# Performance work log

Measured on AMD Instinct MI355X. Metric: run time of the kernel, lower is better.

The kernel has to match this reference:

```python
import jax, jax.numpy as jnp
import numpy as np

DT = 0.01
NJ = 7
GRAV = 9.81
Q_LOWER = jnp.array([-2.9671, -1.8326, -2.9671, -3.1416, -2.9671, -0.0873, -2.9671], jnp.float32)
Q_UPPER = jnp.array([ 2.9671,  1.8326,  2.9671,  0.0,     2.9671,  3.8223,  2.9671], jnp.float32)


def _skew(v):
    z = jnp.zeros((), v.dtype)
    return jnp.stack([jnp.stack([z, -v[2], v[1]]),
                      jnp.stack([v[2], z, -v[0]]),
                      jnp.stack([-v[1], v[0], z])])


def _mot_X(E, r):
    # 6x6 spatial motion transform [[E,0],[-E*skew(r),E]]
    zero = jnp.zeros_like(E)
    top = jnp.concatenate([E, zero], axis=1)
    bot = jnp.concatenate([-E @ _skew(r), E], axis=1)
    return jnp.concatenate([top, bot], axis=0)


def _crm(v):
    # spatial motion cross-product matrix for v=[w;v0]
    Sw, Sv = _skew(v[:3]), _skew(v[3:])
    zero = jnp.zeros_like(Sw)
    top = jnp.concatenate([Sw, zero], axis=1)
    bot = jnp.concatenate([Sv, Sw], axis=1)
    return jnp.concatenate([top, bot], axis=0)


def _step_single(x, u, axes, R_tree, p_tree, I_sp):
    dt_ = x.dtype
    q = jnp.clip(x[:NJ], Q_LOWER.astype(dt_), Q_UPPER.astype(dt_))
    qd = x[NJ:]
    # forward kinematics: per-joint 6x6 child<-parent transforms and motion subspaces
    Xups, Ss = [], []
    eye3 = jnp.eye(3, dtype=dt_)
    for i in range(NJ):
        a = axes[i]
        c, s = jnp.cos(q[i]), jnp.sin(q[i])
        R = c * eye3 + s * _skew(a) + (1.0 - c) * jnp.outer(a, a)  # rodrigues
        Xj = _mot_X(R.T, jnp.zeros(3, dt_))
        Xt = _mot_X(R_tree[i], p_tree[i])
        Xups.append(Xj @ Xt)
        Ss.append(jnp.concatenate([a, jnp.zeros(3, dt_)]))
    # RNEA bias force h (qdd=0, gravity, zero base velocity, identity base pose)
    v_prev = jnp.zeros(6, dt_)
    a_prev = jnp.array([0.0, 0.0, 0.0, 0.0, 0.0, GRAV], dt_)  # a_base = -g trick
    fs = []
    for i in range(NJ):
        vJ = Ss[i] * qd[i]
        v = Xups[i] @ v_prev + vJ
        acc = Xups[i] @ a_prev + _crm(v) @ vJ
        Iv = I_sp[i] @ v
        f = I_sp[i] @ acc - _crm(v).T @ Iv  # crf(v) = -crm(v)^T
        fs.append(f)
        v_prev, a_prev = v, acc
    h = [None] * NJ
    for i in range(NJ - 1, -1, -1):
        h[i] = Ss[i] @ fs[i]
        if i > 0:
            fs[i - 1] = fs[i - 1] + Xups[i].T @ fs[i]
    h = jnp.stack(h)
    # CRBA mass matrix (serial chain, parent(i)=i-1)
    Ic = [I_sp[i] for i in range(NJ)]
    M = jnp.zeros((NJ, NJ), dt_)
    for i in range(NJ - 1, -1, -1):
        if i > 0:
            Ic[i - 1] = Ic[i - 1] + Xups[i].T @ Ic[i] @ Xups[i]
        F = Ic[i] @ Ss[i]
        M = M.at[i, i].set(Ss[i] @ F)
        for j in range(i - 1, -1, -1):
            F = Xups[j + 1].T @ F
            mij = Ss[j] @ F
            M = M.at[i, j].set(mij).at[j, i].set(mij)
    M = M + 1e-8 * jnp.eye(NJ, dtype=dt_)
    qdd = jnp.linalg.solve(M, (u - h)[:, None])[:, 0]
    qd_new = qd + DT * qdd
    q_new = q + DT * qd_new
    return jnp.concatenate([q_new, qd_new])


def setup_inputs() -> dict:
    B = 65536
    key = jax.random.key(0)
    k1, k2 = jax.random.split(key)
    x = jax.random.normal(k1, (B, 14), jnp.float32)
    u = jax.random.normal(k2, (B, 7), jnp.float32)
    rng = np.random.default_rng(0)
    # unit joint axes
    axes = rng.normal(size=(NJ, 3))
    axes = axes / np.linalg.norm(axes, axis=1, keepdims=True)
    # orthonormal fixed parent->child rotations (det +1)
    R_tree = np.empty((NJ, 3, 3))
    for i in range(NJ):
        Q, _ = np.linalg.qr(rng.normal(size=(3, 3)))
        if np.linalg.det(Q) < 0:
            Q[:, 0] = -Q[:, 0]
        R_tree[i] = Q
    p_tree = 0.2 * rng.normal(size=(NJ, 3))
    # SPD 6x6 spatial inertias: [[Ibar, m*Cx],[m*Cx^T, m*I3]]
    I_sp = np.empty((NJ, 6, 6))
    for i in range(NJ):
        m = float(rng.uniform(1.0, 5.0))
        c = 0.05 * rng.normal(size=3)
        Cx = np.array([[0, -c[2], c[1]], [c[2], 0, -c[0]], [-c[1], c[0], 0]])
        A = 0.1 * rng.normal(size=(3, 3))
        Ic_ = A @ A.T + 0.05 * np.eye(3)
        Ibar = Ic_ + m * Cx @ Cx.T
        I_sp[i] = np.block([[Ibar, m * Cx], [m * Cx.T, m * np.eye(3)]])
    return {
        "x": x, "u": u,
        "axes": jnp.asarray(axes, jnp.float32),
        "R_tree": jnp.asarray(R_tree, jnp.float32),
        "p_tree": jnp.asarray(p_tree, jnp.float32),
        "I_sp": jnp.asarray(I_sp, jnp.float32),
    }


def reference(x, u, axes, R_tree, p_tree, I_sp):
    return jax.vmap(_step_single, in_axes=(0, 0, None, None, None, None))(
        x, u, axes, R_tree, p_tree, I_sp)
```

## Files before the change

kernel.cpp:

```cpp
#include <hip/hip_runtime.h>
#include <math.h>

#define NJ 7
#define DTF 0.01f
#define GRAVF 9.81f
#define MIX(i,j) ((i)*((i)+1)/2 + (j))
#define MPAD 29
#define CW 44


__device__ __forceinline__ void cross3(const float* a, const float* b, float* o){
    o[0] = a[1]*b[2] - a[2]*b[1];
    o[1] = a[2]*b[0] - a[0]*b[2];
    o[2] = a[0]*b[1] - a[1]*b[0];
}
__device__ __forceinline__ void mv3(const float* E, const float* x, float* y){
    y[0] = E[0]*x[0] + E[1]*x[1] + E[2]*x[2];
    y[1] = E[3]*x[0] + E[4]*x[1] + E[5]*x[2];
    y[2] = E[6]*x[0] + E[7]*x[1] + E[8]*x[2];
}
__device__ __forceinline__ void mtv3(const float* E, const float* x, float* y){
    y[0] = E[0]*x[0] + E[3]*x[1] + E[6]*x[2];
    y[1] = E[1]*x[0] + E[4]*x[1] + E[7]*x[2];
    y[2] = E[2]*x[0] + E[5]*x[1] + E[8]*x[2];
}
__device__ __forceinline__ void symv(const float* S, const float* x, float* y){
    y[0] = S[0]*x[0] + S[1]*x[1] + S[2]*x[2];
    y[1] = S[1]*x[0] + S[3]*x[1] + S[4]*x[2];
    y[2] = S[2]*x[0] + S[4]*x[1] + S[5]*x[2];
}
__device__ __forceinline__ void mm3(const float* A, const float* B, float* o){
#pragma unroll
    for (int r = 0; r < 3; r++)
#pragma unroll
        for (int c = 0; c < 3; c++)
            o[r*3+c] = A[r*3]*B[c] + A[r*3+1]*B[3+c] + A[r*3+2]*B[6+c];
}
__device__ __forceinline__ void congr(const float* E, const float* X, float* o){
    float t[9];
#pragma unroll
    for (int r = 0; r < 3; r++)
#pragma unroll
        for (int c = 0; c < 3; c++)
            t[r*3+c] = E[r]*X[c] + E[3+r]*X[3+c] + E[6+r]*X[6+c];
    mm3(t, E, o);
}
__device__ __forceinline__ void makeE(const float* __restrict__ cb, float s, float c, float* E){
    float omc = 1.0f - c;
#pragma unroll
    for (int k = 0; k < 9; k++) E[k] = c*cb[k] - s*cb[9+k] + omc*cb[18+k];
}

__global__ void panda_prep(const float* __restrict__ g_ax, const float* __restrict__ g_Rt,
                           const float* __restrict__ g_pt, const float* __restrict__ g_I,
                           float* __restrict__ cst)
{
    int i = threadIdx.x;
    if (i >= NJ) return;
    float a0 = g_ax[i*3], a1 = g_ax[i*3+1], a2 = g_ax[i*3+2];
    const float* R = g_Rt + i*9;
    float* o = cst + i*CW;
#pragma unroll
    for (int k = 0; k < 9; k++) o[k] = R[k];
#pragma unroll
    for (int c = 0; c < 3; c++){
        o[9+c]  = -a2*R[3+c] + a1*R[6+c];
        o[12+c] =  a2*R[c]   - a0*R[6+c];
        o[15+c] = -a1*R[c]   + a0*R[3+c];
        float d =  a0*R[c] + a1*R[3+c] + a2*R[6+c];
        o[18+c] = a0*d; o[21+c] = a1*d; o[24+c] = a2*d;
    }
    o[27]=a0; o[28]=a1; o[29]=a2;
    o[30]=g_pt[i*3]; o[31]=g_pt[i*3+1]; o[32]=g_pt[i*3+2];
    const float* I6 = g_I + i*36;
    o[33]=I6[0];  o[34]=I6[1];  o[35]=I6[2];
    o[36]=I6[7];  o[37]=I6[8];  o[38]=I6[14];
    o[39]=I6[16]; o[40]=I6[5];  o[41]=I6[9];
    o[42]=I6[21];
}

__global__ __launch_bounds__(128)
void panda_step(const float* __restrict__ x, const float* __restrict__ u,
                const float* __restrict__ cst, float* __restrict__ out, int B)
{
    __shared__ float s_M[64*MPAD];

    const int role = threadIdx.x >> 6;
    const int lane = threadIdx.x & 63;
    const int e    = blockIdx.x*64 + lane;
    const bool act = (e < B);

    const float QL[NJ] = {-2.9671f,-1.8326f,-2.9671f,-3.1416f,-2.9671f,-0.0873f,-2.9671f};
    const float QU[NJ] = { 2.9671f, 1.8326f, 2.9671f, 0.0f,    2.9671f, 3.8223f, 2.9671f};

    float q[NJ], qd[NJ], sn[NJ], cs[NJ];
    if (act){
        float xl[14];
        const float2* x2 = (const float2*)(x + e*14);
#pragma unroll
        for (int i = 0; i < 7; i++){ float2 v = x2[i]; xl[2*i] = v.x; xl[2*i+1] = v.y; }
#pragma unroll
        for (int i = 0; i < NJ; i++){
            q[i]  = fminf(fmaxf(xl[i], QL[i]), QU[i]);
            qd[i] = xl[NJ + i];
            __sincosf(q[i], &sn[i], &cs[i]);
        }
    }

    float rhs[NJ];

    if (act && role == 1){
        const float* cb6 = cst + 6*CW;
        float SA[6] = {cb6[33],cb6[34],cb6[35],cb6[36],cb6[37],cb6[38]};
        float hc[3] = {cb6[39],cb6[40],cb6[41]};
        float mc = cb6[42];
        float Fk[NJ][6];
        float Mx[28];
#pragma unroll
        for (int i = NJ-1; i >= 0; i--){
            const float* cb = cst + i*CW;
            const float* a = cb+27;
            const float* p = cb+30;
            symv(SA, a, &Fk[i][0]);
            Fk[i][3] = a[1]*hc[2] - a[2]*hc[1];
            Fk[i][4] = a[2]*hc[0] - a[0]*hc[2];
            Fk[i][5] = a[0]*hc[1] - a[1]*hc[0];
#pragma unroll
            for (int k = i; k < NJ; k++)
                Mx[MIX(k,i)] = a[0]*Fk[k][0] + a[1]*Fk[k][1] + a[2]*Fk[k][2];
            if (i > 0){
                float E[9]; makeE(cb, sn[i], cs[i], E);
                float Af[9] = {SA[0],SA[1],SA[2], SA[1],SA[3],SA[4], SA[2],SA[4],SA[5]};
                float Ap[9]; congr(E, Af, Ap);
                float hr[3]; mtv3(E, hc, hr);
                float hpd = hr[0]*p[0]+hr[1]*p[1]+hr[2]*p[2];
                float ppd = p[0]*p[0]+p[1]*p[1]+p[2]*p[2];
                float dga = 2.0f*hpd + mc*ppd;
                const float* cn = cst + (i-1)*CW;
                SA[0] = Ap[0] - 2.0f*p[0]*hr[0] - mc*p[0]*p[0] + dga + cn[33];
                SA[1] = Ap[1] - p[0]*hr[1] - hr[0]*p[1] - mc*p[0]*p[1] + cn[34];
                SA[2] = Ap[2] - p[0]*hr[2] - hr[0]*p[2] - mc*p[0]*p[2] + cn[35];
                SA[3] = Ap[4] - 2.0f*p[1]*hr[1] - mc*p[1]*p[1] + dga + cn[36];
                SA[4] = Ap[5] - p[1]*hr[2] - hr[1]*p[2] - mc*p[1]*p[2] + cn[37];
                SA[5] = Ap[8] - 2.0f*p[2]*hr[2] - mc*p[2]*p[2] + dga + cn[38];
                hc[0] = hr[0] + mc*p[0] + cn[39];
                hc[1] = hr[1] + mc*p[1] + cn[40];
                hc[2] = hr[2] + mc*p[2] + cn[41];
                mc += cn[42];
#pragma unroll
                for (int k = i; k < NJ; k++){
                    float tm[3], tf[3], cp[3];
                    mtv3(E, &Fk[k][0], tm); mtv3(E, &Fk[k][3], tf);
                    cross3(p, tf, cp);
                    Fk[k][0]=tm[0]+cp[0]; Fk[k][1]=tm[1]+cp[1]; Fk[k][2]=tm[2]+cp[2];
                    Fk[k][3]=tf[0];       Fk[k][4]=tf[1];       Fk[k][5]=tf[2];
                }
            }
        }
#pragma unroll
        for (int j = 0; j < 28; j++) s_M[lane*MPAD + j] = Mx[j];
    }
    else if (act){
#pragma unroll
        for (int i = 0; i < NJ; i++) rhs[i] = u[e*NJ + i];
        float FF[NJ][6];
        float w[3]  = {0.f,0.f,0.f}, vl[3] = {0.f,0.f,0.f};
        float aw[3] = {0.f,0.f,0.f}, av[3] = {0.f,0.f,GRAVF};
#pragma unroll
        for (int i = 0; i < NJ; i++){
            const float* cb = cst + i*CW;
            const float* a = cb+27;
            const float* p = cb+30;
            float E[9]; makeE(cb, sn[i], cs[i], E);
            float qdi = qd[i];
            float tw[3]; mv3(E, w, tw);
            float nw[3] = { tw[0]+a[0]*qdi, tw[1]+a[1]*qdi, tw[2]+a[2]*qdi };
            float cwp[3]; cross3(w, p, cwp);
            float t1[3] = { vl[0]+cwp[0], vl[1]+cwp[1], vl[2]+cwp[2] };
            float nvl[3]; mv3(E, t1, nvl);
            float taw[3]; mv3(E, aw, taw);
            float cna[3]; cross3(nw, a, cna);
            float naw[3] = { taw[0]+qdi*cna[0], taw[1]+qdi*cna[1], taw[2]+qdi*cna[2] };
            float cap[3]; cross3(aw, p, cap);
            float t2[3] = { av[0]+cap[0], av[1]+cap[1], av[2]+cap[2] };
            float tav[3]; mv3(E, t2, tav);
            float cva[3]; cross3(nvl, a, cva);
            float nav[3] = { tav[0]+qdi*cva[0], tav[1]+qdi*cva[1], tav[2]+qdi*cva[2] };
            const float* SAi = cb+33;
            const float* hi  = cb+39;
            float mi = cb[42];
            float Ivt[3], Iat[3], hxv[3], hxa[3];
            symv(SAi, nw, Ivt);  cross3(hi, nvl, hxv);
            symv(SAi, naw, Iat); cross3(hi, nav, hxa);
#pragma unroll
            for (int k = 0; k < 3; k++){ Ivt[k] += hxv[k]; Iat[k] += hxa[k]; }
            float hxw[3], hxaw[3];
            cross3(hi, nw, hxw); cross3(hi, naw, hxaw);
            float Ivb[3] = { mi*nvl[0]-hxw[0], mi*nvl[1]-hxw[1], mi*nvl[2]-hxw[2] };
            float Iab[3] = { mi*nav[0]-hxaw[0], mi*nav[1]-hxaw[1], mi*nav[2]-hxaw[2] };
            float c1[3], c2[3], c3[3];
            cross3(nw, Ivt, c1); cross3(nvl, Ivb, c2); cross3(nw, Ivb, c3);
            FF[i][0] = Iat[0]+c1[0]+c2[0];
            FF[i][1] = Iat[1]+c1[1]+c2[1];
            FF[i][2] = Iat[2]+c1[2]+c2[2];
            FF[i][3] = Iab[0]+c3[0];
            FF[i][4] = Iab[1]+c3[1];
            FF[i][5] = Iab[2]+c3[2];
#pragma unroll
            for (int k = 0; k < 3; k++){ w[k]=nw[k]; vl[k]=nvl[k]; aw[k]=naw[k]; av[k]=nav[k]; }
        }
#pragma unroll
        for (int i = NJ-1; i >= 0; i--){
            const float* cb = cst + i*CW;
            const float* a = cb+27;
            rhs[i] -= a[0]*FF[i][0] + a[1]*FF[i][1] + a[2]*FF[i][2];
            if (i > 0){
                const float* p = cb+30;
                float E[9]; makeE(cb, sn[i], cs[i], E);
                float tm[3], tf[3], cp[3];
                mtv3(E, &FF[i][0], tm); mtv3(E, &FF[i][3], tf);
                cross3(p, tf, cp);
                FF[i-1][0]+=tm[0]+cp[0]; FF[i-1][1]+=tm[1]+cp[1]; FF[i-1][2]+=tm[2]+cp[2];
                FF[i-1][3]+=tf[0];       FF[i-1][4]+=tf[1];       FF[i-1][5]+=tf[2];
            }
        }
    }

    __syncthreads();

    if (act && role == 0){
        float Mx[28];
#pragma unroll
        for (int j = 0; j < 28; j++) Mx[j] = s_M[lane*MPAD + j];
#pragma unroll
        for (int i = 0; i < NJ; i++) Mx[MIX(i,i)] += 1e-8f;

#pragma unroll
        for (int k = 0; k < NJ; k++){
            float d = Mx[MIX(k,k)];
#pragma unroll
            for (int j = 0; j < NJ; j++) if (j < k) d -= Mx[MIX(k,j)]*Mx[MIX(k,j)];
            float linv = __builtin_amdgcn_rsqf(d);
            Mx[MIX(k,k)] = linv;
#pragma unroll
            for (int i = k+1; i < NJ; i++){
                float s2 = Mx[MIX(i,k)];
#pragma unroll
                for (int j = 0; j < NJ; j++) if (j < k) s2 -= Mx[MIX(i,j)]*Mx[MIX(k,j)];
                Mx[MIX(i,k)] = s2 * linv;
            }
        }
        float y[NJ];
#pragma unroll
        for (int i = 0; i < NJ; i++){
            float s2 = rhs[i];
#pragma unroll
            for (int j = 0; j < NJ; j++) if (j < i) s2 -= Mx[MIX(i,j)]*y[j];
            y[i] = s2 * Mx[MIX(i,i)];
        }
        float z[NJ];
#pragma unroll
        for (int i = NJ-1; i >= 0; i--){
            float s2 = y[i];
#pragma unroll
            for (int j = NJ-1; j >= 0; j--) if (j > i) s2 -= Mx[MIX(j,i)]*z[j];
            z[i] = s2 * Mx[MIX(i,i)];
        }

        float o14[14];
#pragma unroll
        for (int i = 0; i < NJ; i++){
            float qdn = qd[i] + DTF*z[i];
            o14[i]      = q[i] + DTF*qdn;
            o14[NJ + i] = qdn;
        }
        float2* o2 = (float2*)(out + e*14);
#pragma unroll
        for (int i = 0; i < 7; i++){ float2 v; v.x = o14[2*i]; v.y = o14[2*i+1]; o2[i] = v; }
    }
}

extern "C" void kernel_launch(void* const* d_in, const int* in_sizes, int n_in,
                              void* d_out, int out_size, void* d_ws, size_t ws_size,
                              hipStream_t stream) {
    const float* x   = (const float*)d_in[0];
    const float* u   = (const float*)d_in[1];
    const float* ax  = (const float*)d_in[2];
    const float* Rt  = (const float*)d_in[3];
    const float* pt  = (const float*)d_in[4];
    const float* Isp = (const float*)d_in[5];
    float* out = (float*)d_out;
    float* cst = (float*)d_ws;
    int B = in_sizes[0] / 14;
    hipLaunchKernelGGL(panda_prep, dim3(1), dim3(64), 0, stream, ax, Rt, pt, Isp, cst);
    int grid = (B + 63) / 64;
    hipLaunchKernelGGL(panda_step, dim3(grid), dim3(128), 0, stream,
                       x, u, cst, out, B);
}
```

Before: 82.87 us.

## Compact constant layout, vectorize loads, cache rotations, move Cholesky to CRBA role

Shrinks the per-joint constant block from 44 to 28 floats and reads it with float4 loads. The rotation is now built on the fly as Rodrigues times R_tree instead of from precomputed basis matrices. The RNEA path keeps the per-joint rotation matrices in registers for the backward pass instead of rebuilding them. The Cholesky factorisation moves from the post-barrier solve warp into the CRBA warp before the shared-memory store, to balance work across the two roles. Doing the 3x3 matrix multiply per joint adds arithmetic, and caching 63 floats per thread raises register pressure.

Measured after the change: 78.42 us. 5.4% less time.

```diff
diff --git a/kernel.cpp b/kernel.cpp
--- a/kernel.cpp
+++ b/kernel.cpp
@@ -6,7 +6,7 @@
 #define GRAVF 9.81f
 #define MIX(i,j) ((i)*((i)+1)/2 + (j))
 #define MPAD 29
-#define CW 44
+#define CW 28
 
 
 __device__ __forceinline__ void cross3(const float* a, const float* b, float* o){
@@ -45,10 +45,41 @@
             t[r*3+c] = E[r]*X[c] + E[3+r]*X[3+c] + E[6+r]*X[6+c];
     mm3(t, E, o);
 }
-__device__ __forceinline__ void makeE(const float* __restrict__ cb, float s, float c, float* E){
+__device__ __forceinline__ void makeE(const float* a, const float* Rt, float s, float c, float* E){
     float omc = 1.0f - c;
-#pragma unroll
-    for (int k = 0; k < 9; k++) E[k] = c*cb[k] - s*cb[9+k] + omc*cb[18+k];
+    float RT[9];
+    RT[0] = c + omc*a[0]*a[0];       RT[1] =  s*a[2] + omc*a[0]*a[1]; RT[2] = -s*a[1] + omc*a[0]*a[2];
+    RT[3] = -s*a[2] + omc*a[1]*a[0]; RT[4] = c + omc*a[1]*a[1];       RT[5] =  s*a[0] + omc*a[1]*a[2];
+    RT[6] =  s*a[1] + omc*a[2]*a[0]; RT[7] = -s*a[0] + omc*a[2]*a[1]; RT[8] = c + omc*a[2]*a[2];
+    mm3(RT, Rt, E);
+}
+__device__ __forceinline__ void loadJ(const float* __restrict__ cst, int i,
+                                      float* Rt, float* a, float* p,
+                                      float* SA, float* h, float& m){
+    const float4* cb4 = (const float4*)(cst + i*CW);
+    float4 c0=cb4[0], c1=cb4[1], c2=cb4[2], c3=cb4[3], c4=cb4[4], c5=cb4[5], c6=cb4[6];
+    Rt[0]=c0.x; Rt[1]=c0.y; Rt[2]=c0.z; Rt[3]=c0.w;
+    Rt[4]=c1.x; Rt[5]=c1.y; Rt[6]=c1.z; Rt[7]=c1.w;
+    Rt[8]=c2.x; a[0]=c2.y; a[1]=c2.z; a[2]=c2.w;
+    p[0]=c3.x; p[1]=c3.y; p[2]=c3.z;
+    SA[0]=c4.x; SA[1]=c4.y; SA[2]=c4.z; SA[3]=c4.w;
+    SA[4]=c5.x; SA[5]=c5.y; h[0]=c5.z; h[1]=c5.w;
+    h[2]=c6.x; m=c6.y;
+}
+__device__ __forceinline__ void loadI(const float* __restrict__ cst, int i,
+                                      float* SA, float* h, float& m){
+    const float4* cb4 = (const float4*)(cst + i*CW);
+    float4 c4=cb4[4], c5=cb4[5], c6=cb4[6];
+    SA[0]=c4.x; SA[1]=c4.y; SA[2]=c4.z; SA[3]=c4.w;
+    SA[4]=c5.x; SA[5]=c5.y; h[0]=c5.z; h[1]=c5.w;
+    h[2]=c6.x; m=c6.y;
+}
+__device__ __forceinline__ void loadAP(const float* __restrict__ cst, int i,
+                                       float* a, float* p){
+    const float4* cb4 = (const float4*)(cst + i*CW);
+    float4 c2=cb4[2], c3=cb4[3];
+    a[0]=c2.y; a[1]=c2.z; a[2]=c2.w;
+    p[0]=c3.x; p[1]=c3.y; p[2]=c3.z;
 }
 
 __global__ void panda_prep(const float* __restrict__ g_ax, const float* __restrict__ g_Rt,
@@ -57,26 +88,16 @@
 {
     int i = threadIdx.x;
     if (i >= NJ) return;
-    float a0 = g_ax[i*3], a1 = g_ax[i*3+1], a2 = g_ax[i*3+2];
-    const float* R = g_Rt + i*9;
     float* o = cst + i*CW;
 #pragma unroll
-    for (int k = 0; k < 9; k++) o[k] = R[k];
-#pragma unroll
-    for (int c = 0; c < 3; c++){
-        o[9+c]  = -a2*R[3+c] + a1*R[6+c];
-        o[12+c] =  a2*R[c]   - a0*R[6+c];
-        o[15+c] = -a1*R[c]   + a0*R[3+c];
-        float d =  a0*R[c] + a1*R[3+c] + a2*R[6+c];
-        o[18+c] = a0*d; o[21+c] = a1*d; o[24+c] = a2*d;
-    }
-    o[27]=a0; o[28]=a1; o[29]=a2;
-    o[30]=g_pt[i*3]; o[31]=g_pt[i*3+1]; o[32]=g_pt[i*3+2];
+    for (int k = 0; k < 9; k++) o[k] = g_Rt[i*9+k];
+    o[9]=g_ax[i*3]; o[10]=g_ax[i*3+1]; o[11]=g_ax[i*3+2];
+    o[12]=g_pt[i*3]; o[13]=g_pt[i*3+1]; o[14]=g_pt[i*3+2]; o[15]=0.f;
     const float* I6 = g_I + i*36;
-    o[33]=I6[0];  o[34]=I6[1];  o[35]=I6[2];
-    o[36]=I6[7];  o[37]=I6[8];  o[38]=I6[14];
-    o[39]=I6[16]; o[40]=I6[5];  o[41]=I6[9];
-    o[42]=I6[21];
+    o[16]=I6[0];  o[17]=I6[1];  o[18]=I6[2];
+    o[19]=I6[7];  o[20]=I6[8];  o[21]=I6[14];
+    o[22]=I6[16]; o[23]=I6[5];  o[24]=I6[9];
+    o[25]=I6[21]; o[26]=0.f; o[27]=0.f;
 }
 
 __global__ __launch_bounds__(128)
@@ -110,17 +131,18 @@
     float rhs[NJ];
 
     if (act && role == 1){
-        const float* cb6 = cst + 6*CW;
-        float SA[6] = {cb6[33],cb6[34],cb6[35],cb6[36],cb6[37],cb6[38]};
-        float hc[3] = {cb6[39],cb6[40],cb6[41]};
-        float mc = cb6[42];
+        float SA[6], hc[3], mc;
+        {
+            float dm; loadI(cst, 6, SA, hc, dm); mc = dm;
+        }
         float Fk[NJ][6];
         float Mx[28];
 #pragma unroll
         for (int i = NJ-1; i >= 0; i--){
-            const float* cb = cst + i*CW;
-            const float* a = cb+27;
-            const float* p = cb+30;
+            float Rt[9], a[3], p[3], SAn[6], hn[3], mn;
+            loadJ(cst, i, Rt, a, p, SAn, hn, mn);
+            float SAm[6], hm[3], mm_;
+            if (i > 0) loadI(cst, i-1, SAm, hm, mm_);
             symv(SA, a, &Fk[i][0]);
             Fk[i][3] = a[1]*hc[2] - a[2]*hc[1];
             Fk[i][4] = a[2]*hc[0] - a[0]*hc[2];
@@ -129,24 +151,23 @@
             for (int k = i; k < NJ; k++)
                 Mx[MIX(k,i)] = a[0]*Fk[k][0] + a[1]*Fk[k][1] + a[2]*Fk[k][2];
             if (i > 0){
-                float E[9]; makeE(cb, sn[i], cs[i], E);
+                float E[9]; makeE(a, Rt, sn[i], cs[i], E);
                 float Af[9] = {SA[0],SA[1],SA[2], SA[1],SA[3],SA[4], SA[2],SA[4],SA[5]};
                 float Ap[9]; congr(E, Af, Ap);
                 float hr[3]; mtv3(E, hc, hr);
                 float hpd = hr[0]*p[0]+hr[1]*p[1]+hr[2]*p[2];
                 float ppd = p[0]*p[0]+p[1]*p[1]+p[2]*p[2];
                 float dga = 2.0f*hpd + mc*ppd;
-                const float* cn = cst + (i-1)*CW;
-                SA[0] = Ap[0] - 2.0f*p[0]*hr[0] - mc*p[0]*p[0] + dga + cn[33];
-                SA[1] = Ap[1] - p[0]*hr[1] - hr[0]*p[1] - mc*p[0]*p[1] + cn[34];
-                SA[2] = Ap[2] - p[0]*hr[2] - hr[0]*p[2] - mc*p[0]*p[2] + cn[35];
-                SA[3] = Ap[4] - 2.0f*p[1]*hr[1] - mc*p[1]*p[1] + dga + cn[36];
-                SA[4] = Ap[5] - p[1]*hr[2] - hr[1]*p[2] - mc*p[1]*p[2] + cn[37];
-                SA[5] = Ap[8] - 2.0f*p[2]*hr[2] - mc*p[2]*p[2] + dga + cn[38];
-                hc[0] = hr[0] + mc*p[0] + cn[39];
-                hc[1] = hr[1] + mc*p[1] + cn[40];
-                hc[2] = hr[2] + mc*p[2] + cn[41];
-                mc += cn[42];
+                SA[0] = Ap[0] - 2.0f*p[0]*hr[0] - mc*p[0]*p[0] + dga + SAm[0];
+                SA[1] = Ap[1] - p[0]*hr[1] - hr[0]*p[1] - mc*p[0]*p[1] + SAm[1];
+                SA[2] = Ap[2] - p[0]*hr[2] - hr[0]*p[2] - mc*p[0]*p[2] + SAm[2];
+                SA[3] = Ap[4] - 2.0f*p[1]*hr[1] - mc*p[1]*p[1] + dga + SAm[3];
+                SA[4] = Ap[5] - p[1]*hr[2] - hr[1]*p[2] - mc*p[1]*p[2] + SAm[4];
+                SA[5] = Ap[8] - 2.0f*p[2]*hr[2] - mc*p[2]*p[2] + dga + SAm[5];
+                hc[0] = hr[0] + mc*p[0] + hm[0];
+                hc[1] = hr[1] + mc*p[1] + hm[1];
+                hc[2] = hr[2] + mc*p[2] + hm[2];
+                mc += mm_;
 #pragma unroll
                 for (int k = i; k < NJ; k++){
                     float tm[3], tf[3], cp[3];
@@ -158,20 +179,38 @@
             }
         }
 #pragma unroll
+        for (int i = 0; i < NJ; i++) Mx[MIX(i,i)] += 1e-8f;
+#pragma unroll
+        for (int k = 0; k < NJ; k++){
+            float d = Mx[MIX(k,k)];
+#pragma unroll
+            for (int j = 0; j < NJ; j++) if (j < k) d -= Mx[MIX(k,j)]*Mx[MIX(k,j)];
+            float linv = __builtin_amdgcn_rsqf(d);
+            Mx[MIX(k,k)] = linv;
+#pragma unroll
+            for (int i2 = k+1; i2 < NJ; i2++){
+                float s2 = Mx[MIX(i2,k)];
+#pragma unroll
+                for (int j = 0; j < NJ; j++) if (j < k) s2 -= Mx[MIX(i2,j)]*Mx[MIX(k,j)];
+                Mx[MIX(i2,k)] = s2 * linv;
+            }
+        }
+#pragma unroll
         for (int j = 0; j < 28; j++) s_M[lane*MPAD + j] = Mx[j];
     }
     else if (act){
 #pragma unroll
         for (int i = 0; i < NJ; i++) rhs[i] = u[e*NJ + i];
+        float Earr[NJ][9];
         float FF[NJ][6];
         float w[3]  = {0.f,0.f,0.f}, vl[3] = {0.f,0.f,0.f};
         float aw[3] = {0.f,0.f,0.f}, av[3] = {0.f,0.f,GRAVF};
 #pragma unroll
         for (int i = 0; i < NJ; i++){
-            const float* cb = cst + i*CW;
-            const float* a = cb+27;
-            const float* p = cb+30;
-            float E[9]; makeE(cb, sn[i], cs[i], E);
+            float Rt[9], a[3], p[3], SAi[6], hi[3], mi;
+            loadJ(cst, i, Rt, a, p, SAi, hi, mi);
+            float* E = &Earr[i][0];
+            makeE(a, Rt, sn[i], cs[i], E);
             float qdi = qd[i];
             float tw[3]; mv3(E, w, tw);
             float nw[3] = { tw[0]+a[0]*qdi, tw[1]+a[1]*qdi, tw[2]+a[2]*qdi };
@@ -186,9 +225,6 @@
             float tav[3]; mv3(E, t2, tav);
             float cva[3]; cross3(nvl, a, cva);
             float nav[3] = { tav[0]+qdi*cva[0], tav[1]+qdi*cva[1], tav[2]+qdi*cva[2] };
-            const float* SAi = cb+33;
-            const float* hi  = cb+39;
-            float mi = cb[42];
             float Ivt[3], Iat[3], hxv[3], hxa[3];
             symv(SAi, nw, Ivt);  cross3(hi, nvl, hxv);
             symv(SAi, naw, Iat); cross3(hi, nav, hxa);
@@ -211,12 +247,11 @@
         }
 #pragma unroll
         for (int i = NJ-1; i >= 0; i--){
-            const float* cb = cst + i*CW;
-            const float* a = cb+27;
+            float a[3], p[3];
+            loadAP(cst, i, a, p);
             rhs[i] -= a[0]*FF[i][0] + a[1]*FF[i][1] + a[2]*FF[i][2];
             if (i > 0){
-                const float* p = cb+30;
-                float E[9]; makeE(cb, sn[i], cs[i], E);
+                const float* E = &Earr[i][0];
                 float tm[3], tf[3], cp[3];
                 mtv3(E, &FF[i][0], tm); mtv3(E, &FF[i][3], tf);
                 cross3(p, tf, cp);
@@ -232,24 +267,6 @@
         float Mx[28];
 #pragma unroll
         for (int j = 0; j < 28; j++) Mx[j] = s_M[lane*MPAD + j];
-#pragma unroll
-        for (int i = 0; i < NJ; i++) Mx[MIX(i,i)] += 1e-8f;
-
-#pragma unroll
-        for (int k = 0; k < NJ; k++){
-            float d = Mx[MIX(k,k)];
-#pragma unroll
-            for (int j = 0; j < NJ; j++) if (j < k) d -= Mx[MIX(k,j)]*Mx[MIX(k,j)];
-            float linv = __builtin_amdgcn_rsqf(d);
-            Mx[MIX(k,k)] = linv;
-#pragma unroll
-            for (int i = k+1; i < NJ; i++){
-                float s2 = Mx[MIX(i,k)];
-#pragma unroll
-                for (int j = 0; j < NJ; j++) if (j < k) s2 -= Mx[MIX(i,j)]*Mx[MIX(k,j)];
-                Mx[MIX(i,k)] = s2 * linv;
-            }
-        }
         float y[NJ];
 #pragma unroll
         for (int i = 0; i < NJ; i++){
@@ -266,7 +283,6 @@
             for (int j = NJ-1; j >= 0; j--) if (j > i) s2 -= Mx[MIX(j,i)]*z[j];
             z[i] = s2 * Mx[MIX(i,i)];
         }
-
         float o14[14];
 #pragma unroll
         for (int i = 0; i < NJ; i++){
```
